# Kernel tuning notes

Measured on AMD Instinct MI355X. Metric: run time of the kernel, lower is better.

Reference implementation:

```python
import jax, jax.numpy as jnp
import numpy as np
from jax import lax

EPS = 1e-20
DN = ('NCHW', 'OIHW', 'NCHW')


def nconv(x, c, w, b, pad):
    """Normalized convolution (Eldesokey NConv2d): conv(data*conf)/conv(conf)."""
    pads = [(pad, pad), (pad, pad)]
    denom = lax.conv_general_dilated(c, w, (1, 1), pads, dimension_numbers=DN)
    nomin = lax.conv_general_dilated(x * c, w, (1, 1), pads, dimension_numbers=DN)
    out = nomin / (denom + EPS) + b[None, :, None, None]
    s = jnp.sum(w, axis=(1, 2, 3))  # per-out-channel kernel sum
    cout = denom / s[None, :, None, None]
    return out, cout


def pool_gather(x, c):
    """2x2 stride-2 max-pool on c; gather x at the argmax locations (vectorized
    replacement for the per-(batch,channel) Python-loop unpool gather)."""
    B, C, H, W = c.shape
    cw = c.reshape(B, C, H // 2, 2, W // 2, 2).transpose(0, 1, 2, 4, 3, 5).reshape(B, C, H // 2, W // 2, 4)
    xw = x.reshape(B, C, H // 2, 2, W // 2, 2).transpose(0, 1, 2, 4, 3, 5).reshape(B, C, H // 2, W // 2, 4)
    idx = jnp.argmax(cw, axis=-1)[..., None]
    c_ds = jnp.take_along_axis(cw, idx, axis=-1)[..., 0]
    x_ds = jnp.take_along_axis(xw, idx, axis=-1)[..., 0]
    return x_ds, c_ds / 4.0


def up2(a):
    """Nearest-neighbor 2x upsample (exact-doubling case of F.interpolate)."""
    return jnp.repeat(jnp.repeat(a, 2, axis=2), 2, axis=3)


def setup_inputs() -> dict:
    key = jax.random.key(0)
    ks = jax.random.split(key, 16)
    C = 32  # (input_channels-1) * mid_channels = 1 * 32
    u = lambda k, sh: jax.random.uniform(k, sh, dtype=jnp.float32) * 0.05
    z = lambda k, sh: jax.random.normal(k, sh, dtype=jnp.float32) * 0.01
    return {
        'x': jax.random.uniform(ks[0], (2, 2, 512, 512), dtype=jnp.float32),
        'w1': u(ks[1], (C, 1, 5, 5)), 'b1': z(ks[2], (C,)),
        'w2': u(ks[3], (C, C, 5, 5)), 'b2': z(ks[4], (C,)),
        'w3': u(ks[5], (C, C, 5, 5)), 'b3': z(ks[6], (C,)),
        'w4': u(ks[7], (C, 2 * C, 3, 3)), 'b4': z(ks[8], (C,)),
        'w5': u(ks[9], (C, 2 * C, 3, 3)), 'b5': z(ks[10], (C,)),
        'w6': u(ks[11], (C, 2 * C, 3, 3)), 'b6': z(ks[12], (C,)),
        'w7': u(ks[13], (1, C, 1, 1)), 'b7': z(ks[14], (1,)),
    }


def reference(x, w1, b1, w2, b2, w3, b3, w4, b4, w5, b5, w6, b6, w7, b7):
    cat = lambda a, b: jnp.concatenate((a, b), axis=1)
    x0 = x[:, 0:1]                                 # data channel
    c0 = jnp.broadcast_to(x[:, 1:2], x0.shape)     # confidence channel repeated
    x1, c1 = nconv(x0, c0, w1, b1, 2)
    x1, c1 = nconv(x1, c1, w2, b2, 2)
    x1, c1 = nconv(x1, c1, w3, b3, 2)
    x1_ds, c1_ds = pool_gather(x1, c1)
    x2_ds, c2_ds = nconv(x1_ds, c1_ds, w2, b2, 2)  # nconv2 weight reuse (as in source)
    x2_ds, c2_ds = nconv(x2_ds, c2_ds, w3, b3, 2)
    x2_dss, c2_dss = pool_gather(x2_ds, c2_ds)
    x3_ds, c3_ds = nconv(x2_dss, c2_dss, w2, b2, 2)
    x3_dss, c3_dss = pool_gather(x3_ds, c3_ds)
    x4_ds, c4_ds = nconv(x3_dss, c3_dss, w2, b2, 2)
    x4, c4 = up2(x4_ds), up2(c4_ds)
    x34_ds, c34_ds = nconv(cat(x3_ds, x4), cat(c3_ds, c4), w4, b4, 1)
    x34, c34 = up2(x34_ds), up2(c34_ds)
    x23_ds, c23_ds = nconv(cat(x2_ds, x34), cat(c2_ds, c34), w5, b5, 1)
    x23, c23 = up2(x23_ds), up2(c23_ds)
    xout, cout = nconv(cat(x23, x1), cat(c23, c1), w6, b6, 1)
    xout, cout = nconv(xout, cout, w7, b7, 0)
    return xout
```

## Files before the change

kernel.cpp:

```cpp
#include <hip/hip_runtime.h>
#include <hip/hip_bf16.h>

#define EPSF 1e-20f

using short8  = __attribute__((ext_vector_type(8))) short;
using float4f = __attribute__((ext_vector_type(4))) float;
typedef const __attribute__((address_space(1))) unsigned int* gas_t;
typedef __attribute__((address_space(3))) unsigned int* las_t;

__device__ __forceinline__ unsigned short f2bf(float f) {
    __hip_bfloat16 h = __float2bfloat16(f);
    return __builtin_bit_cast(unsigned short, h);
}
__device__ __forceinline__ float bf2f(unsigned short u) {
    __hip_bfloat16 h = __builtin_bit_cast(__hip_bfloat16, u);
    return __bfloat162float(h);
}
__device__ __forceinline__ float frcp(float x) { return __builtin_amdgcn_rcpf(x); }

__global__ void wprep_k(const float* __restrict__ w1, const float* __restrict__ w2,
                        const float* __restrict__ w3, const float* __restrict__ w4,
                        const float* __restrict__ w5, const float* __restrict__ w6,
                        float* __restrict__ is1, float* __restrict__ is2,
                        float* __restrict__ is3, float* __restrict__ is4,
                        float* __restrict__ is5, float* __restrict__ is6,
                        unsigned short* __restrict__ wf2, unsigned short* __restrict__ wf3,
                        unsigned short* __restrict__ wf4, unsigned short* __restrict__ wf5,
                        unsigned short* __restrict__ wf6, unsigned short* __restrict__ wf1,
                        unsigned int* __restrict__ zpage) {
    const int tid = threadIdx.x;
    if (blockIdx.x == 0 && tid < 4) zpage[tid] = 0;
    if (blockIdx.x >= 424) {
        int wid = (blockIdx.x - 424) * 4 + (tid >> 6);
        if (wid >= 192) return;
        int task = wid >> 5, co = wid & 31, lane = tid & 63;
        const float* w; int n; float* s;
        switch (task) {
            case 0: w = w1; n = 25;  s = is1; break;
            case 1: w = w2; n = 800; s = is2; break;
            case 2: w = w3; n = 800; s = is3; break;
            case 3: w = w4; n = 576; s = is4; break;
            case 4: w = w5; n = 576; s = is5; break;
            default: w = w6; n = 576; s = is6; break;
        }
        float acc = 0.f;
        for (int i = lane; i < n; i += 64) acc += w[co * n + i];
#pragma unroll
        for (int off = 1; off < 64; off <<= 1) acc += __shfl_xor(acc, off);
        if (lane == 0) s[co] = 1.0f / acc;
        return;
    }
    int idx = blockIdx.x * 256 + tid;
    if (idx < 992) return;
    int r = idx - 992;
    if (r >= 106496) {
        int r2 = r - 106496;
        if (r2 >= 1024) return;
        int j = r2 & 7, lane = (r2 >> 3) & 63, cot = (r2 >> 9) & 1;
        int co = cot * 16 + (lane & 15);
        int tap = (lane >> 4) * 8 + j;
        wf1[r2] = f2bf(tap < 25 ? w1[co * 25 + tap] : 0.f);
        return;
    }
    const float* w; unsigned short* wf; int CIN, KK, cxor;
    if (r < 25600)        {             w = w2; wf = wf2; CIN = 32; KK = 25; cxor = 0;  }
    else if (r < 51200)   { r -= 25600; w = w3; wf = wf3; CIN = 32; KK = 25; cxor = 0;  }
    else if (r < 69632)   { r -= 51200; w = w4; wf = wf4; CIN = 64; KK = 9;  cxor = 0;  }
    else if (r < 88064)   { r -= 69632; w = w5; wf = wf5; CIN = 64; KK = 9;  cxor = 0;  }
    else                  { r -= 88064; w = w6; wf = wf6; CIN = 64; KK = 9;  cxor = 32; }
    int j = r & 7, lane = (r >> 3) & 63, cot = (r >> 9) & 1, ks = r >> 10;
    int phase = ks / KK, tap = ks - phase * KK;
    int co = cot * 16 + (lane & 15);
    int ci = (phase * 32 + (lane >> 4) * 8 + j) ^ cxor;
    wf[r] = f2bf(w[((long)co * CIN + ci) * KK + tap]);
}

__global__ __launch_bounds__(256)
void conv1_k(const float* __restrict__ x, const unsigned short* __restrict__ wf1,
             const float* __restrict__ bias, const float* __restrict__ is_,
             unsigned short* __restrict__ out, int H, int W) {
    constexpr int TIW = 20, TIH = 14, TSZ = TIW * TIH;
    __shared__ unsigned short sp[TSZ], sc_[TSZ];
    __shared__ unsigned short lbb[128 * 32];
    const int tid = threadIdx.x;
    const int wv = tid >> 6, lane = tid & 63, n = lane & 15, q = lane >> 4;
    const int ox0 = blockIdx.x * 16, oy0 = blockIdx.y * 8, b = blockIdx.z;
    const long HW = (long)H * W;
    const float* xd = x + (long)(b * 2) * HW;
    const float* xc = xd + HW;

    for (int i = tid; i < TSZ; i += 256) {
        int py = i / TIW, px = i - py * TIW;
        int gy = oy0 - 2 + py, gx = ox0 - 2 + px;
        float c = 0.f, d = 0.f;
        if (gy >= 0 && gy < H && gx >= 0 && gx < W) {
            long g = (long)gy * W + gx;
            c = xc[g]; d = xd[g];
        }
        sc_[i] = f2bf(c);
        sp[i] = f2bf(d * c);
    }
    __syncthreads();

    int loff[8];
#pragma unroll
    for (int j = 0; j < 8; ++j) {
        int k = q * 8 + j;
        int dy = k / 5, dx = k - 5 * dy;
        loff[j] = dy * TIW + dx;
    }
    short8 a0 = ((const short8*)wf1)[0 * 64 + lane];
    short8 a1 = ((const short8*)wf1)[1 * 64 + lane];

    float4f accP[2][2], accC[2][2];
#pragma unroll
    for (int mt = 0; mt < 2; ++mt) {
        const int rb = (2 * wv + mt) * TIW + n;
        union { short8 v; unsigned short s[8]; } bp, bc;
#pragma unroll
        for (int j = 0; j < 8; ++j) {
            bp.s[j] = sp[rb + loff[j]];
            bc.s[j] = sc_[rb + loff[j]];
        }
        accP[mt][0] = __builtin_amdgcn_mfma_f32_16x16x32_bf16(a0, bp.v, (float4f)0.f, 0, 0, 0);
        accP[mt][1] = __builtin_amdgcn_mfma_f32_16x16x32_bf16(a1, bp.v, (float4f)0.f, 0, 0, 0);
        accC[mt][0] = __builtin_amdgcn_mfma_f32_16x16x32_bf16(a0, bc.v, (float4f)0.f, 0, 0, 0);
        accC[mt][1] = __builtin_amdgcn_mfma_f32_16x16x32_bf16(a1, bc.v, (float4f)0.f, 0, 0, 0);
    }

    float4f b4[2], s4[2];
    b4[0] = *(const float4f*)(bias + q * 4);
    b4[1] = *(const float4f*)(bias + 16 + q * 4);
    s4[0] = *(const float4f*)(is_ + q * 4);
    s4[1] = *(const float4f*)(is_ + 16 + q * 4);

#pragma unroll
    for (int pl = 0; pl < 2; ++pl) {
        __syncthreads();
#pragma unroll
        for (int mt = 0; mt < 2; ++mt) {
            const int pix = (2 * wv + mt) * 16 + n;
#pragma unroll
            for (int ct = 0; ct < 2; ++ct) {
                unsigned int w0, w1v;
                if (pl == 0) {
                    float d0 = accC[mt][ct][0], d1 = accC[mt][ct][1];
                    float d2 = accC[mt][ct][2], d3 = accC[mt][ct][3];
                    float x0 = fmaf(accP[mt][ct][0], frcp(d0 + EPSF), b4[ct][0]) * (d0 * s4[ct][0]);
                    float x1 = fmaf(accP[mt][ct][1], frcp(d1 + EPSF), b4[ct][1]) * (d1 * s4[ct][1]);
                    float x2 = fmaf(accP[mt][ct][2], frcp(d2 + EPSF), b4[ct][2]) * (d2 * s4[ct][2]);
                    float x3 = fmaf(accP[mt][ct][3], frcp(d3 + EPSF), b4[ct][3]) * (d3 * s4[ct][3]);
                    w0 = (unsigned int)f2bf(x0) | ((unsigned int)f2bf(x1) << 16);
                    w1v = (unsigned int)f2bf(x2) | ((unsigned int)f2bf(x3) << 16);
                } else {
                    float c0 = accC[mt][ct][0] * s4[ct][0], c1 = accC[mt][ct][1] * s4[ct][1];
                    float c2 = accC[mt][ct][2] * s4[ct][2], c3 = accC[mt][ct][3] * s4[ct][3];
                    w0 = (unsigned int)f2bf(c0) | ((unsigned int)f2bf(c1) << 16);
                    w1v = (unsigned int)f2bf(c2) | ((unsigned int)f2bf(c3) << 16);
                }
                uint2 v; v.x = w0; v.y = w1v;
                *(uint2*)(lbb + pix * 32 +
                          ((ct * 2 + (q >> 1) + n + (n >> 2)) & 3) * 8 + (q & 1) * 4) = v;
            }
        }
        __syncthreads();
        const unsigned short* obase = out + (long)(b * 2 + pl) * HW * 32;
#pragma unroll
        for (int it = 0; it < 2; ++it) {
            int off = it * 256 + tid;
            int pix = off >> 2, sub = off & 3;
            uint4 v = *(const uint4*)(lbb + pix * 32 + ((sub + pix + (pix >> 2)) & 3) * 8);
            int ry = pix >> 4, rx = pix & 15;
            *(uint4*)(obase + ((long)(oy0 + ry) * W + ox0 + rx) * 32 + sub * 8) = v;
        }
    }
}

template <int KS, int NPH, bool FUSE7, bool POOL>
__global__ __launch_bounds__(256, 4)
void mconv_k(const unsigned short* __restrict__ s1,
             const unsigned short* __restrict__ s2,
             const unsigned short* __restrict__ wf,
             const float* __restrict__ bias, const float* __restrict__ sden,
             unsigned short* __restrict__ out, float* __restrict__ xout,
             const float* __restrict__ w7, const float* __restrict__ b7,
             unsigned short* __restrict__ pout,
             const unsigned int* __restrict__ zpage,
             int H, int W) {
    constexpr int R = KS / 2, KK = KS * KS;
    constexpr int TIH = 8 + KS - 1, TIW = 16 + KS - 1;
    constexpr int PCS = TIH * TIW * 32;
    constexpr int NCH = TIH * TIW * 4;
    __shared__ unsigned short lds[2 * PCS];

    const int tid = threadIdx.x;
    const int wv = tid >> 6, lane = tid & 63, n = lane & 15, q = lane >> 4;
    const int ox0 = blockIdx.x * 16, oy0 = blockIdx.y * 8, b = blockIdx.z;
    const long HW = (long)H * W;

    float4f accP[2][2], accC[2][2];
#pragma unroll
    for (int mt = 0; mt < 2; ++mt)
#pragma unroll
        for (int ct = 0; ct < 2; ++ct) {
            accP[mt][ct] = (float4f)0.f;
            accC[mt][ct] = (float4f)0.f;
        }

    const int PB = (2 * wv) * TIW + n;

    for (int ph = 0; ph < NPH; ++ph) {
        const unsigned short* src = (NPH == 2 && ph == 1) ? s2 : s1;
        if (ph) __syncthreads();
        for (int it = 0; it < (2 * NCH + 255) / 256; ++it) {
            int ch = it * 256 + tid;
            if (ch < 2 * NCH) {
                int pc = ch / NCH, c2 = ch - pc * NCH;
                int pix = c2 >> 2, k8 = c2 & 3;
                int py = pix / TIW, px = pix - py * TIW;
                int gy = oy0 - R + py, gx = ox0 - R + px;
                const unsigned short* ga;
                if (gy >= 0 && gy < H && gx >= 0 && gx < W) {
                    long gi;
                    if (NPH == 2 && ph == 1)
                        gi = ((long)(b * 2 + pc) * (HW >> 2) +
                              (long)(gy >> 1) * (W >> 1) + (gx >> 1)) * 32 + k8 * 8;
                    else
                        gi = ((long)(b * 2 + pc) * HW + (long)gy * W + gx) * 32 + k8 * 8;
                    ga = src + gi;
                } else {
                    ga = (const unsigned short*)zpage;
                }
                __builtin_amdgcn_global_load_lds(
                    (gas_t)ga,
                    (las_t)(lds + (size_t)(it * 256 + wv * 64) * 8),
                    16, 0, 0);
            }
        }
        __syncthreads();
#pragma unroll
        for (int dx = 0; dx < KS; ++dx) {
            short8 a0p, a1p;
#pragma unroll
            for (int r = 0; r < KS + 1; ++r) {
                short8 a0c, a1c;
                if (r < KS) {
                    const int ks = ph * KK + r * KS + dx;
                    a0c = ((const short8*)wf)[(ks * 2 + 0) * 64 + lane];
                    a1c = ((const short8*)wf)[(ks * 2 + 1) * 64 + lane];
                }
                const int p = PB + r * TIW + dx;
                const int off = p * 32 + q * 8;
                short8 bp = *(const short8*)(lds + off);
                short8 bc = *(const short8*)(lds + off + PCS);
                if (r < KS) {
                    accP[0][0] = __builtin_amdgcn_mfma_f32_16x16x32_bf16(a0c, bp, accP[0][0], 0, 0, 0);
                    accP[0][1] = __builtin_amdgcn_mfma_f32_16x16x32_bf16(a1c, bp, accP[0][1], 0, 0, 0);
                    accC[0][0] = __builtin_amdgcn_mfma_f32_16x16x32_bf16(a0c, bc, accC[0][0], 0, 0, 0);
                    accC[0][1] = __builtin_amdgcn_mfma_f32_16x16x32_bf16(a1c, bc, accC[0][1], 0, 0, 0);
                }
                if (r >= 1) {
                    accP[1][0] = __builtin_amdgcn_mfma_f32_16x16x32_bf16(a0p, bp, accP[1][0], 0, 0, 0);
                    accP[1][1] = __builtin_amdgcn_mfma_f32_16x16x32_bf16(a1p, bp, accP[1][1], 0, 0, 0);
                    accC[1][0] = __builtin_amdgcn_mfma_f32_16x16x32_bf16(a0p, bc, accC[1][0], 0, 0, 0);
                    accC[1][1] = __builtin_amdgcn_mfma_f32_16x16x32_bf16(a1p, bc, accC[1][1], 0, 0, 0);
                }
                a0p = a0c; a1p = a1c;
            }
        }
    }

    float4f b4[2], s4[2];
    b4[0] = *(const float4f*)(bias + q * 4);
    b4[1] = *(const float4f*)(bias + 16 + q * 4);
    s4[0] = *(const float4f*)(sden + q * 4);
    s4[1] = *(const float4f*)(sden + 16 + q * 4);

    if (!FUSE7) {
        if (POOL) {
            const int W2 = W >> 1;
            const long HW4 = HW >> 2;
#pragma unroll
            for (int ct = 0; ct < 2; ++ct) {
                unsigned int pw[2], cw[2];
                unsigned short ps[4], cs[4];
#pragma unroll
                for (int r = 0; r < 4; ++r) {
                    float d0 = accC[0][ct][r], d1 = accC[1][ct][r];
                    float c00 = d0 * s4[ct][r];
                    float c10 = d1 * s4[ct][r];
                    float p00 = fmaf(accP[0][ct][r], frcp(d0 + EPSF), b4[ct][r]) * c00;
                    float p10 = fmaf(accP[1][ct][r], frcp(d1 + EPSF), b4[ct][r]) * c10;
                    float c01 = __shfl_xor(c00, 1), c11 = __shfl_xor(c10, 1);
                    float p01 = __shfl_xor(p00, 1), p11 = __shfl_xor(p10, 1);
                    float bc = c00, bp = p00;
                    if (c01 > bc) { bc = c01; bp = p01; }
                    if (c10 > bc) { bc = c10; bp = p10; }
                    if (c11 > bc) { bc = c11; bp = p11; }
                    ps[r] = f2bf(bp * 0.25f);
                    cs[r] = f2bf(bc * 0.25f);
                }
                if (!(n & 1)) {
                    pw[0] = (unsigned int)ps[0] | ((unsigned int)ps[1] << 16);
                    pw[1] = (unsigned int)ps[2] | ((unsigned int)ps[3] << 16);
                    cw[0] = (unsigned int)cs[0] | ((unsigned int)cs[1] << 16);
                    cw[1] = (unsigned int)cs[2] | ((unsigned int)cs[3] << 16);
                    int gy2 = (oy0 >> 1) + wv, gx2 = (ox0 >> 1) + (n >> 1);
                    long pb = ((long)gy2 * W2 + gx2) * 32 + ct * 16 + q * 4;
                    uint2 vp; vp.x = pw[0]; vp.y = pw[1];
                    uint2 vc; vc.x = cw[0]; vc.y = cw[1];
                    *(uint2*)(pout + (long)(b * 2 + 0) * HW4 * 32 + pb) = vp;
                    *(uint2*)(pout + (long)(b * 2 + 1) * HW4 * 32 + pb) = vc;
                }
            }
        }
#pragma unroll
        for (int pl = 0; pl < 2; ++pl) {
            __syncthreads();
#pragma unroll
            for (int mt = 0; mt < 2; ++mt) {
                const int pix = (2 * wv + mt) * 16 + n;
#pragma unroll
                for (int ct = 0; ct < 2; ++ct) {
                    unsigned int w0, w1;
                    if (pl == 0) {
                        float d0 = accC[mt][ct][0], d1 = accC[mt][ct][1];
                        float d2 = accC[mt][ct][2], d3 = accC[mt][ct][3];
                        float x0 = fmaf(accP[mt][ct][0], frcp(d0 + EPSF), b4[ct][0]) * (d0 * s4[ct][0]);
                        float x1 = fmaf(accP[mt][ct][1], frcp(d1 + EPSF), b4[ct][1]) * (d1 * s4[ct][1]);
                        float x2 = fmaf(accP[mt][ct][2], frcp(d2 + EPSF), b4[ct][2]) * (d2 * s4[ct][2]);
                        float x3 = fmaf(accP[mt][ct][3], frcp(d3 + EPSF), b4[ct][3]) * (d3 * s4[ct][3]);
                        w0 = (unsigned int)f2bf(x0) | ((unsigned int)f2bf(x1) << 16);
                        w1 = (unsigned int)f2bf(x2) | ((unsigned int)f2bf(x3) << 16);
                    } else {
                        float c0 = accC[mt][ct][0] * s4[ct][0], c1 = accC[mt][ct][1] * s4[ct][1];
                        float c2 = accC[mt][ct][2] * s4[ct][2], c3 = accC[mt][ct][3] * s4[ct][3];
                        w0 = (unsigned int)f2bf(c0) | ((unsigned int)f2bf(c1) << 16);
                        w1 = (unsigned int)f2bf(c2) | ((unsigned int)f2bf(c3) << 16);
                    }
                    uint2 v; v.x = w0; v.y = w1;
                    *(uint2*)(lds + pix * 32 +
                              ((ct * 2 + (q >> 1) + n + (n >> 2)) & 3) * 8 + (q & 1) * 4) = v;
                }
            }
            __syncthreads();
            const unsigned short* obase = out + (long)(b * 2 + pl) * HW * 32;
#pragma unroll
            for (int it = 0; it < 2; ++it) {
                int off = it * 256 + tid;
                int pix = off >> 2, sub = off & 3;
                uint4 v = *(const uint4*)(lds + pix * 32 + ((sub + pix + (pix >> 2)) & 3) * 8);
                int ry = pix >> 4, rx = pix & 15;
                *(uint4*)(obase + ((long)(oy0 + ry) * W + ox0 + rx) * 32 + sub * 8) = v;
            }
        }
    } else {
        float4f w74[2];
        w74[0] = *(const float4f*)(w7 + q * 4);
        w74[1] = *(const float4f*)(w7 + 16 + q * 4);
        const float b7v = b7[0];
#pragma unroll
        for (int mt = 0; mt < 2; ++mt) {
            float num = 0.f, den = 0.f;
#pragma unroll
            for (int ct = 0; ct < 2; ++ct)
#pragma unroll
                for (int r = 0; r < 4; ++r) {
                    float d = accC[mt][ct][r];
                    float oxv = fmaf(accP[mt][ct][r], frcp(d + EPSF), b4[ct][r]);
                    float oc = d * s4[ct][r];
                    num = fmaf(w74[ct][r], oxv * oc, num);
                    den = fmaf(w74[ct][r], oc, den);
                }
            num += __shfl_xor(num, 16); num += __shfl_xor(num, 32);
            den += __shfl_xor(den, 16); den += __shfl_xor(den, 32);
            if (q == 0) {
                const int oy = oy0 + 2 * wv + mt;
                const int ox = ox0 + n;
                xout[(long)b * HW + (long)oy * W + ox] = fmaf(num, frcp(den + EPSF), b7v);
            }
        }
    }
}

extern "C" void kernel_launch(void* const* d_in, const int* in_sizes, int n_in,
                              void* d_out, int out_size, void* d_ws, size_t ws_size,
                              hipStream_t stream) {
    const float* x  = (const float*)d_in[0];
    const float* w1 = (const float*)d_in[1];
    const float* b1 = (const float*)d_in[2];
    const float* w2 = (const float*)d_in[3];
    const float* b2 = (const float*)d_in[4];
    const float* w3 = (const float*)d_in[5];
    const float* b3 = (const float*)d_in[6];
    const float* w4 = (const float*)d_in[7];
    const float* b4 = (const float*)d_in[8];
    const float* w5 = (const float*)d_in[9];
    const float* b5 = (const float*)d_in[10];
    const float* w6 = (const float*)d_in[11];
    const float* b6 = (const float*)d_in[12];
    const float* w7 = (const float*)d_in[13];
    const float* b7 = (const float*)d_in[14];

    const size_t HW1 = 512 * 512, HW2s = 256 * 256, HW3s = 128 * 128, HW4s = 64 * 64;

    const size_t WARENA = 400000;
    float* fa = (float*)d_ws;
    float *s1 = fa, *s2 = s1 + 32, *s3 = s2 + 32;
    float *s4 = s3 + 32, *s5 = s4 + 32, *s6 = s5 + 32;
    unsigned int* zpage = (unsigned int*)(fa + 192);
    unsigned short* ua = (unsigned short*)((char*)d_ws + 4096);
    unsigned short *wf2 = ua;
    unsigned short *wf3 = wf2 + 25600;
    unsigned short *wf4 = wf3 + 25600;
    unsigned short *wf5 = wf4 + 18432;
    unsigned short *wf6 = wf5 + 18432;
    unsigned short *wf1 = wf6 + 18432;
    unsigned short* buf = (unsigned short*)((char*)d_ws + WARENA);

    const size_t E1 = 2 * 2 * HW1 * 32;
    const size_t E2 = 2 * 2 * HW2s * 32, E3 = 2 * 2 * HW3s * 32, E4 = 2 * 2 * HW4s * 32;
    unsigned short* A = buf;
    unsigned short* B = A + E1;
    unsigned short* P = B;
    unsigned short* Q = P + E2;
    unsigned short* S = Q + E2;
    unsigned short* T = S + E3;
    unsigned short* U = T + E3;
    unsigned short* V = U + E4;

    if (ws_size < WARENA + 2 * E1 * sizeof(unsigned short)) return;

    wprep_k<<<472, 256, 0, stream>>>(w1, w2, w3, w4, w5, w6,
                                     s1, s2, s3, s4, s5, s6,
                                     wf2, wf3, wf4, wf5, wf6, wf1, zpage);

    dim3 blkm(256);
    dim3 g1(32, 64, 2), g2(16, 32, 2), g3(8, 16, 2), g4(4, 8, 2);

    conv1_k<<<g1, blkm, 0, stream>>>(x, wf1, b1, s1, A, 512, 512);
    mconv_k<5, 1, false, false><<<g1, blkm, 0, stream>>>(A, nullptr, wf2, b2, s2, B, nullptr, nullptr, nullptr, nullptr, zpage, 512, 512);
    mconv_k<5, 1, false, true><<<g1, blkm, 0, stream>>>(B, nullptr, wf3, b3, s3, A, nullptr, nullptr, nullptr, P, zpage, 512, 512);

    mconv_k<5, 1, false, false><<<g2, blkm, 0, stream>>>(P, nullptr, wf2, b2, s2, Q, nullptr, nullptr, nullptr, nullptr, zpage, 256, 256);
    mconv_k<5, 1, false, true><<<g2, blkm, 0, stream>>>(Q, nullptr, wf3, b3, s3, P, nullptr, nullptr, nullptr, S, zpage, 256, 256);

    mconv_k<5, 1, false, true><<<g3, blkm, 0, stream>>>(S, nullptr, wf2, b2, s2, T, nullptr, nullptr, nullptr, U, zpage, 128, 128);

    mconv_k<5, 1, false, false><<<g4, blkm, 0, stream>>>(U, nullptr, wf2, b2, s2, V, nullptr, nullptr, nullptr, nullptr, zpage, 64, 64);

    mconv_k<3, 2, false, false><<<g3, blkm, 0, stream>>>(T, V, wf4, b4, s4, S, nullptr, nullptr, nullptr, nullptr, zpage, 128, 128);
    mconv_k<3, 2, false, false><<<g2, blkm, 0, stream>>>(P, S, wf5, b5, s5, Q, nullptr, nullptr, nullptr, nullptr, zpage, 256, 256);
    mconv_k<3, 2, true, false><<<g1, blkm, 0, stream>>>(A, Q, wf6, b6, s6, nullptr, (float*)d_out, w7, b7, nullptr, zpage, 512, 512);
}
```

Measured before the change: 325.2 us.

## Split plane staging to overlap async LDS loads with MFMA taps

Staging of the shared-memory tile now happens one plane at a time (data plane, then confidence plane) instead of loading both before any compute. While one plane's tile is in flight through global_load_lds, the MFMA taps for the previously staged plane run, and for two-phase kernels the second phase's loads are interleaved the same way. The aim is to hide global-to-LDS latency behind matrix work. The cost is extra barriers and reliance on those barriers draining outstanding loads before a region is reused.

```diff
diff --git a/kernel.cpp b/kernel.cpp
--- a/kernel.cpp
+++ b/kernel.cpp
@@ -209,35 +209,36 @@
 
     const int PB = (2 * wv) * TIW + n;
 
-    for (int ph = 0; ph < NPH; ++ph) {
+    auto stage = [&](int pl, int ph) {
         const unsigned short* src = (NPH == 2 && ph == 1) ? s2 : s1;
-        if (ph) __syncthreads();
-        for (int it = 0; it < (2 * NCH + 255) / 256; ++it) {
+        for (int it = 0; it < (NCH + 255) / 256; ++it) {
             int ch = it * 256 + tid;
-            if (ch < 2 * NCH) {
-                int pc = ch / NCH, c2 = ch - pc * NCH;
-                int pix = c2 >> 2, k8 = c2 & 3;
+            if (ch < NCH) {
+                int pix = ch >> 2, k8 = ch & 3;
                 int py = pix / TIW, px = pix - py * TIW;
                 int gy = oy0 - R + py, gx = ox0 - R + px;
                 const unsigned short* ga;
                 if (gy >= 0 && gy < H && gx >= 0 && gx < W) {
                     long gi;
                     if (NPH == 2 && ph == 1)
-                        gi = ((long)(b * 2 + pc) * (HW >> 2) +
+                        gi = ((long)(b * 2 + pl) * (HW >> 2) +
                               (long)(gy >> 1) * (W >> 1) + (gx >> 1)) * 32 + k8 * 8;
                     else
-                        gi = ((long)(b * 2 + pc) * HW + (long)gy * W + gx) * 32 + k8 * 8;
+                        gi = ((long)(b * 2 + pl) * HW + (long)gy * W + gx) * 32 + k8 * 8;
                     ga = src + gi;
                 } else {
                     ga = (const unsigned short*)zpage;
                 }
                 __builtin_amdgcn_global_load_lds(
                     (gas_t)ga,
-                    (las_t)(lds + (size_t)(it * 256 + wv * 64) * 8),
+                    (las_t)(lds + (size_t)pl * PCS + (size_t)(it * 256 + wv * 64) * 8),
                     16, 0, 0);
             }
         }
-        __syncthreads();
+    };
+
+    auto taps = [&](float4f (&acc)[2][2], int region, int ph) {
+        const int base = region * PCS;
 #pragma unroll
         for (int dx = 0; dx < KS; ++dx) {
             short8 a0p, a1p;
@@ -249,25 +250,35 @@
                     a0c = ((const short8*)wf)[(ks * 2 + 0) * 64 + lane];
                     a1c = ((const short8*)wf)[(ks * 2 + 1) * 64 + lane];
                 }
-                const int p = PB + r * TIW + dx;
-                const int off = p * 32 + q * 8;
-                short8 bp = *(const short8*)(lds + off);
-                short8 bc = *(const short8*)(lds + off + PCS);
+                short8 bb = *(const short8*)(lds + base + (PB + r * TIW + dx) * 32 + q * 8);
                 if (r < KS) {
-                    accP[0][0] = __builtin_amdgcn_mfma_f32_16x16x32_bf16(a0c, bp, accP[0][0], 0, 0, 0);
-                    accP[0][1] = __builtin_amdgcn_mfma_f32_16x16x32_bf16(a1c, bp, accP[0][1], 0, 0, 0);
-                    accC[0][0] = __builtin_amdgcn_mfma_f32_16x16x32_bf16(a0c, bc, accC[0][0], 0, 0, 0);
-                    accC[0][1] = __builtin_amdgcn_mfma_f32_16x16x32_bf16(a1c, bc, accC[0][1], 0, 0, 0);
+                    acc[0][0] = __builtin_amdgcn_mfma_f32_16x16x32_bf16(a0c, bb, acc[0][0], 0, 0, 0);
+                    acc[0][1] = __builtin_amdgcn_mfma_f32_16x16x32_bf16(a1c, bb, acc[0][1], 0, 0, 0);
                 }
                 if (r >= 1) {
-                    accP[1][0] = __builtin_amdgcn_mfma_f32_16x16x32_bf16(a0p, bp, accP[1][0], 0, 0, 0);
-                    accP[1][1] = __builtin_amdgcn_mfma_f32_16x16x32_bf16(a1p, bp, accP[1][1], 0, 0, 0);
-                    accC[1][0] = __builtin_amdgcn_mfma_f32_16x16x32_bf16(a0p, bc, accC[1][0], 0, 0, 0);
-                    accC[1][1] = __builtin_amdgcn_mfma_f32_16x16x32_bf16(a1p, bc, accC[1][1], 0, 0, 0);
+                    acc[1][0] = __builtin_amdgcn_mfma_f32_16x16x32_bf16(a0p, bb, acc[1][0], 0, 0, 0);
+                    acc[1][1] = __builtin_amdgcn_mfma_f32_16x16x32_bf16(a1p, bb, acc[1][1], 0, 0, 0);
                 }
                 a0p = a0c; a1p = a1c;
             }
         }
+    };
+
+    stage(0, 0);
+    __syncthreads();
+    stage(1, 0);
+    taps(accP, 0, 0);
+    __syncthreads();
+    if (NPH == 2) {
+        stage(0, 1);
+        taps(accC, 1, 0);
+        __syncthreads();
+        stage(1, 1);
+        taps(accP, 0, 1);
+        __syncthreads();
+        taps(accC, 1, 1);
+    } else {
+        taps(accC, 1, 0);
     }
 
     float4f b4[2], s4[2];
```

Measured after the change: 370.8 us. +14.0%, slower.
